# Optimization experiments

Hardware: AMD Instinct MI355X
Metric: run time of the kernel (lower is better)

## Reference

```python
import jax, jax.numpy as jnp
import numpy as np

VAR_NUM = [29, 2, 1, 6, 7, 59, 1, 24, 76, 711, 3, 9, 1]  # sums to 929
TEMP = 0.8
EPS = 1e-20


def setup_inputs() -> dict:
    key = jax.random.key(0)
    ks = jax.random.split(key, 8)
    B, D, H, O = 32768, 128, 1024, 929
    s = lambda n: 1.0 / np.sqrt(n)
    return {
        "x": jax.random.normal(ks[0], (B, D), jnp.float32),
        "W1": jax.random.uniform(ks[1], (D, H), jnp.float32, -s(D), s(D)),
        "b1": jax.random.uniform(ks[2], (H,), jnp.float32, -s(D), s(D)),
        "W2": jax.random.uniform(ks[3], (H, H), jnp.float32, -s(H), s(H)),
        "b2": jax.random.uniform(ks[4], (H,), jnp.float32, -s(H), s(H)),
        "W3": jax.random.uniform(ks[5], (H, O), jnp.float32, -s(H), s(H)),
        "b3": jax.random.uniform(ks[6], (O,), jnp.float32, -s(H), s(H)),
        "u": jax.random.uniform(ks[7], (B, O), jnp.float32),  # U(0,1) gumbel base noise
    }


def reference(x, W1, b1, W2, b2, W3, b3, u):
    h = jax.nn.elu(x @ W1 + b1)          # [B, H]
    h = jax.nn.sigmoid(h @ W2 + b2)      # [B, H]
    logits = h @ W3 + b3                 # [B, 929]
    g = -jnp.log(-jnp.log(u + EPS) + EPS)  # gumbel noise, [B, 929]
    outs = []
    off = 0
    for n in VAR_NUM:  # fixed 13 segments
        seg = logits[:, off:off + n]
        if n == 1:
            outs.append(seg)  # passthrough for continuous columns
        else:
            y = (seg + g[:, off:off + n]) / TEMP
            outs.append(jax.nn.softmax(y, axis=-1))
        off += n
    return jnp.concatenate(outs, axis=1)  # [B, 929]
```

## Files before the change

### kernel.cpp

```cpp
#include <hip/hip_runtime.h>
#include <hip/hip_bf16.h>
#include <stdint.h>

#define GEPS 1e-20f

typedef __bf16 bf16x8 __attribute__((ext_vector_type(8)));
typedef float  f32x4  __attribute__((ext_vector_type(4)));

typedef const __attribute__((address_space(1))) uint32_t* gptr32;
typedef __attribute__((address_space(3))) uint32_t* lptr32;

__device__ __forceinline__ void load_lds16(const void* g, void* l) {
    __builtin_amdgcn_global_load_lds((gptr32)g, (lptr32)l, 16, 0, 0);
}

__device__ __forceinline__ uint16_t f2bf(float v) {
    __hip_bfloat16 b = __float2bfloat16(v);
    return *(uint16_t*)&b;
}
__device__ __forceinline__ float bf2f(uint16_t b) {
    uint32_t u = (uint32_t)b << 16;
    return __builtin_bit_cast(float, u);
}

#define LN2   0.69314718056f
#define LOG2E 1.44269504089f
__device__ __forceinline__ float fast_log(float x) { return __builtin_amdgcn_logf(x) * LN2; }
__device__ __forceinline__ float fast_exp(float x) { return __builtin_amdgcn_exp2f(x * LOG2E); }
__device__ __forceinline__ float fast_exp2(float x) { return __builtin_amdgcn_exp2f(x); }
__device__ __forceinline__ float fast_rcp(float x)  { return __builtin_amdgcn_rcpf(x); }

__device__ __forceinline__ void store_val(uint16_t* C, size_t idx, float v) { C[idx] = f2bf(v); }
__device__ __forceinline__ void store_val(float* C, size_t idx, float v)    { C[idx] = v; }

__global__ void cast_bf16(const float* __restrict__ in, uint16_t* __restrict__ out, int n) {
    int i = (blockIdx.x * blockDim.x + threadIdx.x) * 4;
    if (i < n) {
        float4 v = *(const float4*)(in + i);
        ushort4 o;
        o.x = f2bf(v.x); o.y = f2bf(v.y); o.z = f2bf(v.z); o.w = f2bf(v.w);
        *(ushort4*)(out + i) = o;
    }
}

__global__ void transpose_cast(const float* __restrict__ W, uint16_t* __restrict__ Wt,
                               int K, int N, int Npad) {
    __shared__ float tile[64][65];
    const int k0 = blockIdx.y * 64, n0 = blockIdx.x * 64;
    const int tx = threadIdx.x & 63, ty = threadIdx.x >> 6;
    for (int r = ty; r < 64; r += 4) {
        int n = n0 + tx;
        tile[r][tx] = (n < N) ? W[(size_t)(k0 + r) * N + n] : 0.f;
    }
    __syncthreads();
    for (int r = ty; r < 64; r += 4) {
        Wt[(size_t)(n0 + r) * K + k0 + tx] = f2bf(tile[tx][r]);
    }
}

template<int ACT, typename OutT, bool SNG>
__global__ __launch_bounds__(256)
void gemm_bt(const uint16_t* __restrict__ A, const uint16_t* __restrict__ Bt,
             const float* __restrict__ bias, OutT* __restrict__ C,
             float* __restrict__ sngl,
             int K, int Nout, int ldc) {
    __shared__ __align__(16) uint16_t As[128 * 32];
    __shared__ __align__(16) uint16_t Bs[128 * 32];

    const int t    = threadIdx.x;
    const int wave = t >> 6, lane = t & 63;

    const int nbx = gridDim.x;
    const int bid = blockIdx.y * nbx + blockIdx.x;
    const int xcd = bid & 7;
    const int s   = bid >> 3;
    const int nidx = s % nbx;
    const int midx = xcd * (gridDim.y >> 3) + s / nbx;

    const int m0 = midx * 128, n0 = nidx * 128;
    const int wm = (wave >> 1) * 64, wn = (wave & 1) * 64;
    const int quad = lane >> 4;
    const int qk   = quad * 8;
    const int r15  = lane & 15;

    f32x4 acc[4][4] = {};

    const uint16_t* Ag = A  + (size_t)m0 * K;
    const uint16_t* Bg = Bt + (size_t)n0 * K;

    for (int k0 = 0; k0 < K; k0 += 32) {
        __syncthreads();
        #pragma unroll
        for (int rd = 0; rd < 2; ++rd) {
            int c = t + rd * 256;
            int row = c >> 2, kc = (c & 3) * 8;
            load_lds16(Ag + (size_t)row * K + k0 + kc, &As[c * 8]);
            load_lds16(Bg + (size_t)row * K + k0 + kc, &Bs[c * 8]);
        }
        __syncthreads();

        bf16x8 a[4], b[4];
        #pragma unroll
        for (int i = 0; i < 4; ++i)
            a[i] = *(const bf16x8*)&As[(wm + i * 16 + r15) * 32 + qk];
        #pragma unroll
        for (int i = 0; i < 4; ++i)
            b[i] = *(const bf16x8*)&Bs[(wn + i * 16 + r15) * 32 + qk];

        #pragma unroll
        for (int mi = 0; mi < 4; ++mi)
            #pragma unroll
            for (int ni = 0; ni < 4; ++ni)
                acc[mi][ni] = __builtin_amdgcn_mfma_f32_16x16x32_bf16(
                    a[mi], b[ni], acc[mi][ni], 0, 0, 0);
    }

    #pragma unroll
    for (int ni = 0; ni < 4; ++ni) {
        int col = n0 + wn + ni * 16 + r15;
        if (col < Nout) {
            float bv = bias[col];
            bool is_sng = SNG && (col == 31 || col == 104 || col == 928);
            #pragma unroll
            for (int mi = 0; mi < 4; ++mi) {
                #pragma unroll
                for (int r = 0; r < 4; ++r) {
                    int row = m0 + wm + mi * 16 + quad * 4 + r;
                    float v = acc[mi][ni][r] + bv;
                    if (ACT == 1) v = (v > 0.f) ? v : (fast_exp(v) - 1.f);
                    else if (ACT == 2) v = fast_rcp(1.f + fast_exp(-v));
                    store_val(C, (size_t)row * ldc + col, v);
                    if constexpr (SNG) {
                        if (is_sng) sngl[(size_t)row * 929 + col] = v;
                    }
                }
            }
        }
    }
}

#define NEG_BIG (-1e30f)
#define Y2_LG   1.8033688011f

__device__ __forceinline__ float y2_col(const uint16_t* __restrict__ rlg,
                                        const float* __restrict__ ru, int c) {
    float l2u   = __builtin_amdgcn_logf(ru[c] + GEPS);
    float inner = fmaf(-LN2, l2u, GEPS);
    float l2i   = __builtin_amdgcn_logf(inner);
    return fmaf(Y2_LG, bf2f(rlg[c]), -1.25f * l2i);
}

template<int N, int OFF>
__device__ __forceinline__ void seg_small(const uint16_t* __restrict__ rlg,
                                          const float* __restrict__ ru,
                                          float* __restrict__ rout, int l32) {
    static_assert(N <= 32, "seg_small needs N<=32");
    constexpr int GS = (N <= 2) ? 2 : (N <= 4) ? 4 : (N <= 8) ? 8 : (N <= 16) ? 16 : 32;
    const bool act = l32 < N;
    const int  c   = OFF + l32;
    float y = act ? y2_col(rlg, ru, c) : NEG_BIG;
    float m = y;
    #pragma unroll
    for (int o = 1; o < GS; o <<= 1) m = fmaxf(m, __shfl_xor(m, o, 64));
    float e = act ? fast_exp2(y - m) : 0.f;
    float s = e;
    #pragma unroll
    for (int o = 1; o < GS; o <<= 1) s += __shfl_xor(s, o, 64);
    if (act) rout[c] = e * fast_rcp(s);
}

template<int N, int OFF>
__device__ __forceinline__ void seg_wide(const uint16_t* __restrict__ rlg,
                                         const float* __restrict__ ru,
                                         float* __restrict__ rout, int lane) {
    constexpr int IT = (N + 63) / 64;
    float y[IT];
    float m = NEG_BIG;
    #pragma unroll
    for (int i = 0; i < IT; ++i) {
        const int j = i * 64 + lane;
        y[i] = (j < N) ? y2_col(rlg, ru, OFF + j) : NEG_BIG;
        m = fmaxf(m, y[i]);
    }
    #pragma unroll
    for (int o = 1; o < 64; o <<= 1) m = fmaxf(m, __shfl_xor(m, o, 64));
    float s = 0.f;
    #pragma unroll
    for (int i = 0; i < IT; ++i) {
        float e = fast_exp2(y[i] - m);
        y[i] = e;
        s += e;
    }
    #pragma unroll
    for (int o = 1; o < 64; o <<= 1) s += __shfl_xor(s, o, 64);
    const float inv = fast_rcp(s);
    #pragma unroll
    for (int i = 0; i < IT; ++i) {
        const int j = i * 64 + lane;
        if (j < N) rout[OFF + j] = y[i] * inv;
    }
}

__global__ __launch_bounds__(256)
void gumbel_epilogue(const uint16_t* __restrict__ lg, float* __restrict__ out,
                     const float* __restrict__ u, int B) {
    const int wave = threadIdx.x >> 6, lane = threadIdx.x & 63;
    const int l32  = lane & 31, half = lane >> 5;
    const int rowA = blockIdx.x * 8 + wave * 2;
    if (rowA >= B) return;

    const size_t baseA = (size_t)rowA * 929;
    const size_t baseB = baseA + 929;
    const size_t baseH = half ? baseB : baseA;

    const uint16_t* lgH = lg  + baseH;
    const float*    uH  = u   + baseH;
    float*          oH  = out + baseH;
    seg_small<29,   0>(lgH, uH, oH, l32);
    seg_small< 2,  29>(lgH, uH, oH, l32);
    seg_small< 6,  32>(lgH, uH, oH, l32);
    seg_small< 7,  38>(lgH, uH, oH, l32);
    seg_small<24, 105>(lgH, uH, oH, l32);
    seg_small< 3, 916>(lgH, uH, oH, l32);
    seg_small< 9, 919>(lgH, uH, oH, l32);

    const uint16_t* lgA = lg + baseA; const float* uA = u + baseA; float* oA = out + baseA;
    const uint16_t* lgB = lg + baseB; const float* uB = u + baseB; float* oB = out + baseB;
    seg_wide< 59,  45>(lgA, uA, oA, lane);
    seg_wide< 59,  45>(lgB, uB, oB, lane);
    seg_wide< 76, 129>(lgA, uA, oA, lane);
    seg_wide< 76, 129>(lgB, uB, oB, lane);
    seg_wide<711, 205>(lgA, uA, oA, lane);
    seg_wide<711, 205>(lgB, uB, oB, lane);
}

extern "C" void kernel_launch(void* const* d_in, const int* in_sizes, int n_in,
                              void* d_out, int out_size, void* d_ws, size_t ws_size,
                              hipStream_t stream) {
    const float* x  = (const float*)d_in[0];
    const float* W1 = (const float*)d_in[1];
    const float* b1 = (const float*)d_in[2];
    const float* W2 = (const float*)d_in[3];
    const float* b2 = (const float*)d_in[4];
    const float* W3 = (const float*)d_in[5];
    const float* b3 = (const float*)d_in[6];
    const float* u  = (const float*)d_in[7];
    float* out = (float*)d_out;

    const int B = 32768, D = 128, H = 1024, O = 929, OP = 1024;

    char* ws = (char*)d_ws;
    uint16_t* xb  = (uint16_t*)ws; ws += (size_t)B * D * 2;
    uint16_t* w1t = (uint16_t*)ws; ws += (size_t)H * D * 2;
    uint16_t* w2t = (uint16_t*)ws; ws += (size_t)H * H * 2;
    uint16_t* w3t = (uint16_t*)ws; ws += (size_t)OP * H * 2;
    uint16_t* h1  = (uint16_t*)ws; ws += (size_t)B * H * 2;
    uint16_t* h2  = (uint16_t*)ws; ws += (size_t)B * H * 2;
    uint16_t* lg  = h1;

    cast_bf16<<<(B * D / 4 + 255) / 256, 256, 0, stream>>>(x, xb, B * D);
    transpose_cast<<<dim3(H / 64, D / 64), 256, 0, stream>>>(W1, w1t, D, H, H);
    transpose_cast<<<dim3(H / 64, H / 64), 256, 0, stream>>>(W2, w2t, H, H, H);
    transpose_cast<<<dim3(OP / 64, H / 64), 256, 0, stream>>>(W3, w3t, H, O, OP);

    gemm_bt<1, uint16_t, false><<<dim3(H / 128, B / 128), 256, 0, stream>>>(
        xb, w1t, b1, h1, nullptr, D, H, H);
    gemm_bt<2, uint16_t, false><<<dim3(H / 128, B / 128), 256, 0, stream>>>(
        h1, w2t, b2, h2, nullptr, H, H, H);
    gemm_bt<0, uint16_t, true><<<dim3(OP / 128, B / 128), 256, 0, stream>>>(
        h2, w3t, b3, lg, out, H, O, O);

    gumbel_epilogue<<<B / 8, 256, 0, stream>>>(lg, out, u, B);
}
```

Before: 507.1 us.

## Add 256x256 pipelined GEMM kernel for the two large K=1024 layers

Introduces a 512-thread GEMM with 256x256 block tiles that double-buffers A/B tiles in 128KB of LDS via direct global-to-LDS loads. It interleaves staged loads with MFMA quarters under explicit barriers, waitcnts and wave priority, and remaps block ids across XCDs for L2 locality. The second and third layers now use it instead of the 128x128 kernel, aiming for more reuse per byte loaded and hidden memory latency. The cost is heavy LDS use, which may limit occupancy, and a fragile hand-written schedule.

```diff
diff --git a/kernel.cpp b/kernel.cpp
--- a/kernel.cpp
+++ b/kernel.cpp
@@ -139,6 +139,171 @@
     }
 }
 
+#define BARRIER() asm volatile("s_barrier" ::: "memory")
+#define LGKM0()   do { asm volatile("s_waitcnt lgkmcnt(0)" ::: "memory"); \
+                       __builtin_amdgcn_sched_barrier(0); } while (0)
+#define VMW4()    asm volatile("s_waitcnt vmcnt(4)" ::: "memory")
+#define VMW0()    asm volatile("s_waitcnt vmcnt(0)" ::: "memory")
+#define PRIO1()   __builtin_amdgcn_s_setprio(1)
+#define PRIO0()   __builtin_amdgcn_s_setprio(0)
+
+template<int ACT, typename OutT, bool SNG, int K>
+__global__ __launch_bounds__(512, 2)
+void gemm256(const uint16_t* __restrict__ A, const uint16_t* __restrict__ Bt,
+             const float* __restrict__ bias, OutT* __restrict__ C,
+             float* __restrict__ sngl, int Nout, int ldc) {
+    constexpr int NT = K / 64;
+    constexpr int NI = NT / 2;
+    constexpr int KB = K * 2;
+    __shared__ __align__(16) char lds[131072];
+    constexpr int AOFF0 = 0, BOFF0 = 32768, AOFF1 = 65536, BOFF1 = 98304;
+
+    const int t = threadIdx.x;
+    const int wave = t >> 6, lane = t & 63;
+    const int quad = lane >> 4, r15 = lane & 15;
+    const int wm = (wave >> 2) * 128, wn = (wave & 3) * 64;
+
+    const int nbx = gridDim.x;
+    const int bid = blockIdx.y * nbx + blockIdx.x;
+    const int xcd = bid & 7;
+    const int sb  = bid >> 3;
+    const int nidx = sb % nbx;
+    const int midx = xcd * (gridDim.y >> 3) + sb / nbx;
+    const int m0 = midx * 256, n0 = nidx * 256;
+
+    const int srow = t >> 3;
+    const int scb  = ((t & 7) ^ (srow & 7)) << 4;
+    const char* Asrc = (const char*)A  + (size_t)(m0 + srow) * KB + scb;
+    const char* Bsrc = (const char*)Bt + (size_t)(n0 + srow) * KB + scb;
+
+    const int sx   = (r15 & 7) << 4;
+    const int cb0  = (quad * 16) ^ sx;
+    const int cb1  = (64 + quad * 16) ^ sx;
+    const int aRow = (wm + r15) * 128;
+    const int bRow = (wn + r15) * 128;
+
+    f32x4 acc[8][4] = {};
+    bf16x8 a[4][2], b[4][2];
+
+#define STG(src, half, tile, ldsOff)                                                      \
+    do {                                                                                  \
+        const char* _s = (src) + (size_t)((half) * 128) * KB + (size_t)(tile) * 128;      \
+        load_lds16(_s,                   &lds[(ldsOff) + (half) * 16384 + t * 16]);       \
+        load_lds16(_s + (size_t)64 * KB, &lds[(ldsOff) + (half) * 16384 + 8192 + t * 16]);\
+    } while (0)
+
+    auto ldA = [&](int buf, int mh) {
+        #pragma unroll
+        for (int mi = 0; mi < 4; ++mi) {
+            const int base = buf * 65536 + aRow + (mh * 4 + mi) * 2048;
+            a[mi][0] = *(const bf16x8*)&lds[base + cb0];
+            a[mi][1] = *(const bf16x8*)&lds[base + cb1];
+        }
+    };
+    auto ldB = [&](int buf, int nh) {
+        #pragma unroll
+        for (int ni = 0; ni < 2; ++ni) {
+            const int base = buf * 65536 + 32768 + bRow + (nh * 2 + ni) * 2048;
+            b[nh * 2 + ni][0] = *(const bf16x8*)&lds[base + cb0];
+            b[nh * 2 + ni][1] = *(const bf16x8*)&lds[base + cb1];
+        }
+    };
+    auto mfmaQ = [&](int mlo, int nlo) {
+        #pragma unroll
+        for (int mi = 0; mi < 4; ++mi)
+            #pragma unroll
+            for (int ni = 0; ni < 2; ++ni)
+                #pragma unroll
+                for (int kk = 0; kk < 2; ++kk)
+                    acc[mlo + mi][nlo + ni] = __builtin_amdgcn_mfma_f32_16x16x32_bf16(
+                        a[mi][kk], b[nlo + ni][kk], acc[mlo + mi][nlo + ni], 0, 0, 0);
+    };
+
+    STG(Bsrc, 0, 0, BOFF0); STG(Bsrc, 1, 0, BOFF0);
+    STG(Asrc, 0, 0, AOFF0); STG(Asrc, 1, 0, AOFF0);
+    STG(Bsrc, 0, 1, BOFF1); STG(Bsrc, 1, 1, BOFF1);
+    VMW4(); BARRIER();
+
+    #pragma unroll 1
+    for (int ki = 0; ki < NI; ++ki) {
+        const int t1 = 2 * ki + 1;
+        const int p0 = (2 * ki + 2) & (NT - 1);
+        const int p1 = (2 * ki + 3) & (NT - 1);
+
+        ldA(0, 0); ldB(0, 0);
+        STG(Asrc, 0, t1, AOFF1);
+        BARRIER(); LGKM0();
+        PRIO1(); mfmaQ(0, 0); PRIO0();
+        BARRIER();
+
+        ldB(0, 1);
+        STG(Asrc, 1, t1, AOFF1);
+        BARRIER(); LGKM0();
+        PRIO1(); mfmaQ(0, 2); PRIO0();
+        BARRIER();
+
+        ldA(0, 1);
+        STG(Bsrc, 0, p0, BOFF0);
+        BARRIER(); LGKM0();
+        PRIO1(); mfmaQ(4, 2); PRIO0();
+        BARRIER();
+
+        STG(Bsrc, 1, p0, BOFF0);
+        BARRIER();
+        PRIO1(); mfmaQ(4, 0); PRIO0();
+        VMW4(); BARRIER();
+
+        ldA(1, 0); ldB(1, 0);
+        STG(Asrc, 0, p0, AOFF0);
+        BARRIER(); LGKM0();
+        PRIO1(); mfmaQ(0, 0); PRIO0();
+        BARRIER();
+
+        ldB(1, 1);
+        STG(Asrc, 1, p0, AOFF0);
+        BARRIER(); LGKM0();
+        PRIO1(); mfmaQ(0, 2); PRIO0();
+        BARRIER();
+
+        ldA(1, 1);
+        STG(Bsrc, 0, p1, BOFF1);
+        BARRIER(); LGKM0();
+        PRIO1(); mfmaQ(4, 2); PRIO0();
+        BARRIER();
+
+        STG(Bsrc, 1, p1, BOFF1);
+        BARRIER();
+        PRIO1(); mfmaQ(4, 0); PRIO0();
+        VMW4(); BARRIER();
+    }
+    VMW0();
+
+#undef STG
+
+    #pragma unroll
+    for (int ni = 0; ni < 4; ++ni) {
+        const int col = n0 + wn + ni * 16 + r15;
+        if (col < Nout) {
+            const float bv = bias[col];
+            const bool is_sng = SNG && (col == 31 || col == 104 || col == 928);
+            #pragma unroll
+            for (int mi = 0; mi < 8; ++mi) {
+                #pragma unroll
+                for (int r = 0; r < 4; ++r) {
+                    const int row = m0 + wm + mi * 16 + quad * 4 + r;
+                    float v = acc[mi][ni][r] + bv;
+                    if (ACT == 1) v = (v > 0.f) ? v : (fast_exp(v) - 1.f);
+                    else if (ACT == 2) v = fast_rcp(1.f + fast_exp(-v));
+                    store_val(C, (size_t)row * ldc + col, v);
+                    if constexpr (SNG) {
+                        if (is_sng) sngl[(size_t)row * 929 + col] = v;
+                    }
+                }
+            }
+        }
+    }
+}
+
 #define NEG_BIG (-1e30f)
 #define Y2_LG   1.8033688011f
 
@@ -265,10 +430,10 @@
 
     gemm_bt<1, uint16_t, false><<<dim3(H / 128, B / 128), 256, 0, stream>>>(
         xb, w1t, b1, h1, nullptr, D, H, H);
-    gemm_bt<2, uint16_t, false><<<dim3(H / 128, B / 128), 256, 0, stream>>>(
-        h1, w2t, b2, h2, nullptr, H, H, H);
-    gemm_bt<0, uint16_t, true><<<dim3(OP / 128, B / 128), 256, 0, stream>>>(
-        h2, w3t, b3, lg, out, H, O, O);
+    gemm256<2, uint16_t, false, 1024><<<dim3(H / 256, B / 256), 512, 0, stream>>>(
+        h1, w2t, b2, h2, nullptr, H, H);
+    gemm256<0, uint16_t, true, 1024><<<dim3(OP / 256, B / 256), 512, 0, stream>>>(
+        h2, w3t, b3, lg, out, O, O);
 
     gumbel_epilogue<<<B / 8, 256, 0, stream>>>(lg, out, u, B);
 }
```

Result: faster. 486.6 us (-4.0%).
